# Kernel tuning notes

Hardware: AMD Instinct MI355X
Metric: run time of the kernel (lower is better)

## Reference

```python
import jax, jax.numpy as jnp
import numpy as np

E = 1_000_000
D_IN = 64
D_OUT = 64
N_TYPES = 8


def setup_inputs() -> dict:
    key = jax.random.key(0)
    k1, k2, k3, k4 = jax.random.split(key, 4)
    edge_features = jax.random.normal(k1, (E, D_IN), dtype=jnp.float32)
    edge_types = jax.random.randint(k2, (E,), 0, N_TYPES, dtype=jnp.int64)
    # per-type Linear params: W[t] is [in, out], b[t] is [out]
    W = jax.random.normal(k3, (N_TYPES, D_IN, D_OUT), dtype=jnp.float32) * (1.0 / np.sqrt(D_IN))
    b = jax.random.normal(k4, (N_TYPES, D_OUT), dtype=jnp.float32) * 0.01
    return {"edge_features": edge_features, "edge_types": edge_types, "W": W, "b": b}


def reference(edge_features, edge_types, W, b):
    # Per-edge-type Linear + ReLU, scattered back by type mask.
    # Loop is over the small fixed set of edge types (structurally distinct
    # weight matrices), not over the edge data dimension.
    out = jnp.zeros((edge_features.shape[0], D_OUT), dtype=edge_features.dtype)
    for t in range(N_TYPES):
        y = jax.nn.relu(edge_features @ W[t] + b[t])  # [E, D_OUT]
        mask = (edge_types == t)[:, None]
        out = jnp.where(mask, y, out)
    return out
```

## Files before the change

### kernel.cpp

```cpp
#include <hip/hip_runtime.h>
#include <stdint.h>

#define D 64
#define NT 8
#define CHUNK 1024
#define BLOCK 256

typedef __attribute__((ext_vector_type(8))) short short8;
typedef __attribute__((ext_vector_type(4))) float f32x4;

__device__ __forceinline__ unsigned short f2bf(float f) {
    union { float f; unsigned u; } v; v.f = f;
    unsigned u = v.u;
    unsigned r = (u + 0x7FFFu + ((u >> 16) & 1u)) >> 16;
    return (unsigned short)r;
}

__global__ void __launch_bounds__(BLOCK)
edge_mlp_kernel(const float* __restrict__ ef, const int* __restrict__ types,
                const float* __restrict__ W, const float* __restrict__ Bv,
                float* __restrict__ out, int E)
{
    __shared__ unsigned short bucket[CHUNK];
    __shared__ unsigned cnt[NT];
    __shared__ unsigned startoff[NT];
    __shared__ unsigned cursor[NT];

    const int tid  = threadIdx.x;
    const int base = blockIdx.x * CHUNK;
    const int clen = min(CHUNK, E - base);
    if (clen <= 0) return;

    if (tid < NT) cnt[tid] = 0;
    __syncthreads();

    int myt[CHUNK / BLOCK];
#pragma unroll
    for (int i = 0; i < CHUNK / BLOCK; ++i) {
        int idx = tid + i * BLOCK;
        int t = -1;
        if (idx < clen) {
            t = types[base + idx];
            atomicAdd(&cnt[t], 1u);
        }
        myt[i] = t;
    }
    __syncthreads();
    if (tid == 0) {
        unsigned s = 0;
        for (int t = 0; t < NT; ++t) { startoff[t] = s; cursor[t] = s; s += cnt[t]; }
    }
    __syncthreads();
#pragma unroll
    for (int i = 0; i < CHUNK / BLOCK; ++i) {
        if (myt[i] >= 0) {
            unsigned pos = atomicAdd(&cursor[myt[i]], 1u);
            bucket[pos] = (unsigned short)(tid + i * BLOCK);
        }
    }
    __syncthreads();

    const int wave = tid >> 6;
    const int lane = tid & 63;
    const int n = lane & 15;
    const int g = lane >> 4;

    for (int ti = 0; ti < 2; ++ti) {
        const int t = wave * 2 + ti;
        const unsigned V  = cnt[t];
        if (V == 0) continue;
        const unsigned bs = startoff[t];

        short8 bf[2][4];
        const float* Wt = W + (size_t)t * D * D;
#pragma unroll
        for (int kb = 0; kb < 2; ++kb) {
#pragma unroll
            for (int nb = 0; nb < 4; ++nb) {
                short8 f;
#pragma unroll
                for (int j = 0; j < 8; ++j) {
                    float w = Wt[(size_t)(kb * 32 + g * 8 + j) * D + nb * 16 + n];
                    f[j] = (short)f2bf(w);
                }
                bf[kb][nb] = f;
            }
        }
        float bias[4];
#pragma unroll
        for (int nb = 0; nb < 4; ++nb) bias[nb] = Bv[t * D + nb * 16 + n];

        const unsigned nbatch = (V + 15u) >> 4;
        for (unsigned b = 0; b < nbatch; ++b) {
            const unsigned p0 = b << 4;
            unsigned pm = p0 + (unsigned)n;
            if (pm >= V) pm = V - 1;
            const int gidx = base + (int)bucket[bs + pm];
            const float* row = ef + (size_t)gidx * D;

            f32x4 a0 = *(const f32x4*)(row + g * 8);
            f32x4 a1 = *(const f32x4*)(row + g * 8 + 4);
            f32x4 a2 = *(const f32x4*)(row + 32 + g * 8);
            f32x4 a3 = *(const f32x4*)(row + 32 + g * 8 + 4);

            short8 fa0, fa1;
#pragma unroll
            for (int j = 0; j < 4; ++j) {
                fa0[j]     = (short)f2bf(a0[j]);
                fa0[j + 4] = (short)f2bf(a1[j]);
                fa1[j]     = (short)f2bf(a2[j]);
                fa1[j + 4] = (short)f2bf(a3[j]);
            }

            f32x4 acc[4];
#pragma unroll
            for (int nb = 0; nb < 4; ++nb) acc[nb] = (f32x4){0.f, 0.f, 0.f, 0.f};

#pragma unroll
            for (int nb = 0; nb < 4; ++nb) {
                acc[nb] = __builtin_amdgcn_mfma_f32_16x16x32_bf16(fa0, bf[0][nb], acc[nb], 0, 0, 0);
                acc[nb] = __builtin_amdgcn_mfma_f32_16x16x32_bf16(fa1, bf[1][nb], acc[nb], 0, 0, 0);
            }

#pragma unroll
            for (int r = 0; r < 4; ++r) {
                const int rowpos = g * 4 + r;
                const int sidx = __shfl(gidx, rowpos);
                if (p0 + (unsigned)rowpos < V) {
                    float* orow = out + (size_t)sidx * D;
#pragma unroll
                    for (int nb = 0; nb < 4; ++nb) {
                        float v = acc[nb][r] + bias[nb];
                        orow[nb * 16 + n] = v > 0.f ? v : 0.f;
                    }
                }
            }
        }
    }
}

extern "C" void kernel_launch(void* const* d_in, const int* in_sizes, int n_in,
                              void* d_out, int out_size, void* d_ws, size_t ws_size,
                              hipStream_t stream) {
    const float* ef    = (const float*)d_in[0];
    const int*   types = (const int*)d_in[1];
    const float* W     = (const float*)d_in[2];
    const float* Bv    = (const float*)d_in[3];
    float* out = (float*)d_out;
    const int E = in_sizes[1];
    const int grid = (E + CHUNK - 1) / CHUNK;
    hipLaunchKernelGGL(edge_mlp_kernel, dim3(grid), dim3(BLOCK), 0, stream,
                       ef, types, W, Bv, out, E);
}
```

Before: 446.3 us.

## Stage chunk rows as bf16 in LDS with coalesced loads before typed MFMA

Each block now loads its whole chunk of edge rows from global memory in a coalesced, contiguous pattern, converts them to bf16 once and stores them in padded shared memory. The per-type MFMA loop then reads A fragments from LDS through the bucket index instead of gathering scattered rows from global memory, and prefetches the next bucket index one batch ahead. CHUNK is halved to 512 so the 72KB staging buffer fits in LDS. The trade-off is heavier LDS use per block, which limits occupancy, and twice as many blocks, each paying the W fragment setup cost.

Measured after the change: 455.6 us. +2.1%, slower.

```diff
diff --git a/kernel.cpp b/kernel.cpp
--- a/kernel.cpp
+++ b/kernel.cpp
@@ -3,8 +3,9 @@
 
 #define D 64
 #define NT 8
-#define CHUNK 1024
+#define CHUNK 512
 #define BLOCK 256
+#define RSTRIDE 144
 
 typedef __attribute__((ext_vector_type(8))) short short8;
 typedef __attribute__((ext_vector_type(4))) float f32x4;
@@ -21,6 +22,7 @@
                 const float* __restrict__ W, const float* __restrict__ Bv,
                 float* __restrict__ out, int E)
 {
+    __shared__ __align__(16) unsigned char rowsmem[CHUNK * RSTRIDE];
     __shared__ unsigned short bucket[CHUNK];
     __shared__ unsigned cnt[NT];
     __shared__ unsigned startoff[NT];
@@ -45,7 +47,25 @@
         }
         myt[i] = t;
     }
+
+#pragma unroll
+    for (int i = 0; i < (CHUNK * D / 4) / BLOCK; ++i) {
+        const int p = tid + i * BLOCK;
+        const int e = p * 4;
+        const int r = e >> 6;
+        const int c = e & 63;
+        if (r < clen) {
+            f32x4 v = *(const f32x4*)(ef + (size_t)(base + r) * D + c);
+            unsigned long long pk =
+                  (unsigned long long)f2bf(v[0])
+                | ((unsigned long long)f2bf(v[1]) << 16)
+                | ((unsigned long long)f2bf(v[2]) << 32)
+                | ((unsigned long long)f2bf(v[3]) << 48);
+            *(unsigned long long*)(rowsmem + (size_t)r * RSTRIDE + c * 2) = pk;
+        }
+    }
     __syncthreads();
+
     if (tid == 0) {
         unsigned s = 0;
         for (int t = 0; t < NT; ++t) { startoff[t] = s; cursor[t] = s; s += cnt[t]; }
@@ -91,31 +111,25 @@
         for (int nb = 0; nb < 4; ++nb) bias[nb] = Bv[t * D + nb * 16 + n];
 
         const unsigned nbatch = (V + 15u) >> 4;
+
+        unsigned pm0 = min((unsigned)n, V - 1u);
+        unsigned lidx = bucket[bs + pm0];
+
         for (unsigned b = 0; b < nbatch; ++b) {
             const unsigned p0 = b << 4;
-            unsigned pm = p0 + (unsigned)n;
-            if (pm >= V) pm = V - 1;
-            const int gidx = base + (int)bucket[bs + pm];
-            const float* row = ef + (size_t)gidx * D;
+            const unsigned cur = lidx;
+            unsigned nxt = min(p0 + 16u + (unsigned)n, V - 1u);
+            lidx = bucket[bs + nxt];
 
-            f32x4 a0 = *(const f32x4*)(row + g * 8);
-            f32x4 a1 = *(const f32x4*)(row + g * 8 + 4);
-            f32x4 a2 = *(const f32x4*)(row + 32 + g * 8);
-            f32x4 a3 = *(const f32x4*)(row + 32 + g * 8 + 4);
+            const int gidx = base + (int)cur;
 
-            short8 fa0, fa1;
-#pragma unroll
-            for (int j = 0; j < 4; ++j) {
-                fa0[j]     = (short)f2bf(a0[j]);
-                fa0[j + 4] = (short)f2bf(a1[j]);
-                fa1[j]     = (short)f2bf(a2[j]);
-                fa1[j + 4] = (short)f2bf(a3[j]);
-            }
+            const unsigned short* rp = (const unsigned short*)(rowsmem + (size_t)cur * RSTRIDE);
+            short8 fa0 = *(const short8*)(rp + g * 8);
+            short8 fa1 = *(const short8*)(rp + 32 + g * 8);
 
             f32x4 acc[4];
 #pragma unroll
             for (int nb = 0; nb < 4; ++nb) acc[nb] = (f32x4){0.f, 0.f, 0.f, 0.f};
-
 #pragma unroll
             for (int nb = 0; nb < 4; ++nb) {
                 acc[nb] = __builtin_amdgcn_mfma_f32_16x16x32_bf16(fa0, bf[0][nb], acc[nb], 0, 0, 0);
```
